# Kernel tuning notes

Measured on AMD Instinct MI355X. Metric: run time of the kernel, lower is better.

Reference implementation:

```python
import jax, jax.numpy as jnp
import numpy as np

ALPHA = 0.2      # LeakyReLU negative slope
NEG_INF = -9e15  # mask value from the original code

def setup_inputs() -> dict:
    key = jax.random.key(0)
    k1, k2, k3, k4 = jax.random.split(key, 4)
    B, M, F_IN, F_OUT = 16, 2048, 128, 64
    h = jax.random.normal(k1, (B, M, F_IN), dtype=jnp.float32)
    adj = jax.random.randint(k2, (B, M, M), 0, 2, dtype=jnp.int32)
    W = jax.random.normal(k3, (F_IN, F_OUT), dtype=jnp.float32) * 0.1
    a = jax.random.normal(k4, (2 * F_OUT, 1), dtype=jnp.float32) * 0.1
    return {"h": h, "adj": adj, "W": W, "a": a}

def reference(h, adj, W, a):
    # h: [B,M,Fin], adj: [B,M,M], W: [Fin,E], a: [2E,1]
    Wh = jnp.matmul(h, W)                      # [B,M,E]
    E = Wh.shape[-1]
    a1, a2 = a[:E, 0], a[E:, 0]
    # decompose a^T [Wh_i || Wh_j] = (Wh_i . a1) + (Wh_j . a2)
    f1 = Wh @ a1                               # [B,M] (source/query term)
    f2 = Wh @ a2                               # [B,M] (target/key term)
    e = jax.nn.leaky_relu(f1[:, :, None] + f2[:, None, :], negative_slope=ALPHA)  # [B,M,M]
    scores = jnp.where(adj > 0, e, NEG_INF)
    attn = jax.nn.softmax(scores, axis=-1)     # [B,M,M]  (dropout p=0 / eval mode)
    h_prime = jnp.matmul(attn, Wh)             # [B,M,E]
    return jax.nn.elu(h_prime)                 # concat=True branch
```

## Files before the change

### kernel.cpp

```cpp
#include <hip/hip_runtime.h>


#define M_     2048
#define FIN_   128
#define F_     64
#define ALPHA_ 0.2f
#define HS_    132
#define WT_    132
#define MS_    68

typedef float  float4_ __attribute__((ext_vector_type(4)));
typedef short  short8  __attribute__((ext_vector_type(8)));
typedef int    int4_   __attribute__((ext_vector_type(4)));
typedef unsigned int u32x4 __attribute__((ext_vector_type(4)));
typedef unsigned short u16;
typedef unsigned int   u32;

static __device__ __forceinline__ u32 cvtpk(float lo, float hi) {
    u32 r;
    asm("v_cvt_pk_bf16_f32 %0, %1, %2" : "=v"(r) : "v"(lo), "v"(hi));
    return r;
}

static __device__ __forceinline__ int4_ ntload4(const int* p) {
    return __builtin_nontemporal_load((const int4_*)p);
}

__global__ __launch_bounds__(256, 4) void k_prep(
    const float* __restrict__ h, const float* __restrict__ W,
    const float* __restrict__ a, u16* __restrict__ hbf,
    float* __restrict__ f1all, float* __restrict__ f2all)
{
    __shared__ float a_s[2 * F_];
    __shared__ float wa1[FIN_], wa2[FIN_];
    __shared__ float hs[32 * HS_];

    const int tid = threadIdx.x;
    const u32 bid = blockIdx.x;
    const u32 lg  = (bid & 7) * 128 + (bid >> 3);
    const int b   = lg >> 6;
    const int t   = lg & 63;

    if (tid < 128) a_s[tid] = a[tid];

    const int tok = tid >> 3, f0 = (tid & 7) * 16;
    const float* hp = h + ((size_t)(b * M_ + t * 32 + tok)) * FIN_ + f0;
    float4_ x0 = *(const float4_*)hp;
    float4_ x1 = *(const float4_*)(hp + 4);
    float4_ x2 = *(const float4_*)(hp + 8);
    float4_ x3 = *(const float4_*)(hp + 12);
    __syncthreads();

    if (tid < FIN_) {
        float s1 = 0.f, s2 = 0.f;
#pragma unroll 8
        for (int n = 0; n < F_; ++n) {
            float wv = W[tid * F_ + n];
            s1 += wv * a_s[n];
            s2 += wv * a_s[F_ + n];
        }
        wa1[tid] = s1;
        wa2[tid] = s2;
    }

    float* hr = hs + tok * HS_ + f0;
    *(float4_*)(hr)      = x0;
    *(float4_*)(hr + 4)  = x1;
    *(float4_*)(hr + 8)  = x2;
    *(float4_*)(hr + 12) = x3;
    __syncthreads();

    {
        const int l = tid & 63, lc = l & 15, q = l >> 4;
        const int nt0 = (tid >> 6) * 2;
        u32x4* ob = (u32x4*)hbf + ((size_t)(b * 64 + t)) * 8 * 64;
#pragma unroll
        for (int ni = 0; ni < 2; ++ni) {
            const int nt = nt0 + ni;
            const float* cp = hs + (q * 8) * HS_ + nt * 16 + lc;
            u32x4 wv;
            wv[0] = cvtpk(cp[0 * HS_], cp[1 * HS_]);
            wv[1] = cvtpk(cp[2 * HS_], cp[3 * HS_]);
            wv[2] = cvtpk(cp[4 * HS_], cp[5 * HS_]);
            wv[3] = cvtpk(cp[6 * HS_], cp[7 * HS_]);
            ob[nt * 64 + l] = wv;
        }
    }

    {
        const int r = tid >> 3, k0 = (tid & 7) * 16;
        const float* rp = hs + r * HS_ + k0;
        float s1 = 0.f, s2 = 0.f;
#pragma unroll
        for (int k = 0; k < 16; ++k) {
            s1 += rp[k] * wa1[k0 + k];
            s2 += rp[k] * wa2[k0 + k];
        }
        s1 += __shfl_xor(s1, 1, 64); s2 += __shfl_xor(s2, 1, 64);
        s1 += __shfl_xor(s1, 2, 64); s2 += __shfl_xor(s2, 2, 64);
        s1 += __shfl_xor(s1, 4, 64); s2 += __shfl_xor(s2, 4, 64);
        if ((tid & 7) == 0) {
            f1all[b * M_ + t * 32 + r] = s1;
            f2all[b * M_ + t * 32 + r] = s2;
        }
    }
}

__global__ __launch_bounds__(256, 4) void k_pack(
    const int* __restrict__ adj, u32* __restrict__ mask)
{
    const int l = threadIdx.x & 63;
    u32 s = blockIdx.x * 4 + (threadIdx.x >> 6);
#pragma unroll 4
    for (int it = 0; it < 32; ++it, s += 8192) {
        int4_ v = ntload4(adj + (size_t)s * 256 + l * 4);
        u32 m = ((v[0] > 0 ? 1u : 0u) | (v[1] > 0 ? 2u : 0u)
               | (v[2] > 0 ? 4u : 0u) | (v[3] > 0 ? 8u : 0u)) << ((l & 7) * 4);
        m |= __shfl_xor(m, 1, 64);
        m |= __shfl_xor(m, 2, 64);
        m |= __shfl_xor(m, 4, 64);
        if ((l & 7) == 0) mask[s * 8 + (l >> 3)] = m;
    }
}

__global__ __launch_bounds__(256, 2) void k_main(
    const u32* __restrict__ mask, const u16* __restrict__ hbf,
    const float* __restrict__ f1all, const float* __restrict__ f2all,
    const float* __restrict__ W, float* __restrict__ out)
{
    __shared__ char  dyn[41984];
    __shared__ float dens[64];

    u32x4* lbuf = (u32x4*)dyn;
    float* f2s  = (float*)(dyn + 16384);
    u32*   mlds = (u32*)(dyn + 24576);
    float* Tsum = (float*)dyn;

    const int tid  = threadIdx.x;
    const int w    = tid >> 6;
    const int l    = tid & 63;
    const int lc   = l & 15;
    const int quad = l >> 4;

    const u32 bid = blockIdx.x;
    const u32 lg  = (bid & 7) * 64 + (bid >> 3);
    const int b   = lg >> 5;
    const int i0  = (lg & 31) * 64;

    {
        const int o = tid * 8;
        float4_ v0 = *(const float4_*)(f2all + b * M_ + o);
        float4_ v1 = *(const float4_*)(f2all + b * M_ + o + 4);
        *(float4_*)(f2s + o)     = v0;
        *(float4_*)(f2s + o + 4) = v1;
    }
    {
        const u32* mrow = mask + ((size_t)(b * M_ + i0)) * 64;
#pragma unroll
        for (int c = 0; c < 4; ++c) {
            const int gw = c * 1024 + tid * 4;
            u32x4 v = *(const u32x4*)(mrow + gw);
            *(u32x4*)(mlds + (gw >> 6) * MS_ + (gw & 63)) = v;
        }
    }

    const float f1r = f1all[b * M_ + i0 + w * 16 + lc];
    const u32x4* hbs = (const u32x4*)hbf + (size_t)b * 32768;
    const u32* mrd = mlds + (w * 16 + lc) * MS_;
    const int  msh = quad * 8;

    u32x4 sA0, sA1, sB0, sB1;
    sA0 = hbs[tid];
    sA1 = hbs[256 + tid];
    lbuf[tid]       = sA0;
    lbuf[256 + tid] = sA1;
    sB0 = hbs[512 + tid];
    sB1 = hbs[512 + 256 + tid];

    __syncthreads();

    float denacc = 0.f;
    float4_ acc[8];
#pragma unroll
    for (int nt = 0; nt < 8; ++nt) acc[nt] = (float4_){0.f, 0.f, 0.f, 0.f};

#define SC(GE, GO, BE, BO, IDX)                                 \
        {                                                       \
            float xe = f1r + (GE); xe = fmaxf(xe, ALPHA_ * xe); \
            float xo = f1r + (GO); xo = fmaxf(xo, ALPHA_ * xo); \
            float ee = (mq & (1u << (BE))) ? __expf(xe) : 0.f;  \
            float eo = (mq & (1u << (BO))) ? __expf(xo) : 0.f;  \
            u32 pk = cvtpk(ee, eo);                             \
            d += __uint_as_float(pk << 16);                     \
            d += __uint_as_float(pk & 0xFFFF0000u);             \
            pw[IDX] = pk;                                       \
        }

#define STAGE(T, L0, L1, W0, W1)                                              \
    {                                                                         \
        const int tl = ((T) + 2 < 64) ? (T) + 2 : 63;                         \
        L0 = hbs[tl * 512 + tid];                                             \
        L1 = hbs[tl * 512 + 256 + tid];                                       \
        __builtin_amdgcn_sched_barrier(0);                                    \
        const u32x4* lc_ = lbuf + ((T) & 1) * 512;                            \
        u32x4 bb[8];                                                          \
        _Pragma("unroll")                                                     \
        for (int nt = 0; nt < 8; ++nt) bb[nt] = lc_[nt * 64 + l];             \
        const u32 mq = mrd[T] >> msh;                                         \
        float4_ g0 = *(const float4_*)(f2s + (T) * 32 + quad * 8);            \
        float4_ g1 = *(const float4_*)(f2s + (T) * 32 + quad * 8 + 4);        \
        u32x4 pw;                                                             \
        float d = 0.f;                                                        \
        SC(g0[0], g0[1], 0, 1, 0)                                             \
        SC(g0[2], g0[3], 2, 3, 1)                                             \
        SC(g1[0], g1[1], 4, 5, 2)                                             \
        SC(g1[2], g1[3], 6, 7, 3)                                             \
        denacc += d;                                                          \
        const short8 af = __builtin_bit_cast(short8, pw);                     \
        _Pragma("unroll")                                                     \
        for (int nt = 0; nt < 8; ++nt)                                        \
            acc[nt] = __builtin_amdgcn_mfma_f32_16x16x32_bf16(                \
                af, __builtin_bit_cast(short8, bb[nt]), acc[nt], 0, 0, 0);    \
        __builtin_amdgcn_sched_barrier(0);                                    \
        u32x4* ln_ = lbuf + (((T) + 1) & 1) * 512;                            \
        ln_[tid]       = W0;                                                  \
        ln_[256 + tid] = W1;                                                  \
        asm volatile("s_waitcnt lgkmcnt(0)" ::: "memory");                    \
        __builtin_amdgcn_s_barrier();                                         \
        __builtin_amdgcn_sched_barrier(0);                                    \
    }

    for (int o2 = 0; o2 < 32; ++o2) {
        STAGE(2 * o2,     sA0, sA1, sB0, sB1)
        STAGE(2 * o2 + 1, sB0, sB1, sA0, sA1)
    }
#undef STAGE
#undef SC

    denacc += __shfl_xor(denacc, 16, 64);
    denacc += __shfl_xor(denacc, 32, 64);
    if (quad == 0) dens[w * 16 + lc] = denacc;
    __syncthreads();

#pragma unroll
    for (int nt = 0; nt < 8; ++nt)
#pragma unroll
        for (int mm = 0; mm < 4; ++mm)
            Tsum[(w * 16 + quad * 4 + mm) * WT_ + nt * 16 + lc] = acc[nt][mm];
    __syncthreads();

#pragma unroll
    for (int rr = 0; rr < 2; ++rr) {
        const int r  = (tid >> 3) + rr * 32;
        const int n0 = (tid & 7) * 8;
        const float den  = dens[r];
        const float rden = (den > 0.f) ? (1.f / den) : 0.f;
        float u[8];
#pragma unroll
        for (int nn = 0; nn < 8; ++nn) u[nn] = 0.f;
#pragma unroll 4
        for (int k = 0; k < FIN_; ++k) {
            const float tv = Tsum[r * WT_ + k];
            float4_ wv0 = *(const float4_*)(W + k * F_ + n0);
            float4_ wv1 = *(const float4_*)(W + k * F_ + n0 + 4);
            u[0] += tv * wv0[0]; u[1] += tv * wv0[1];
            u[2] += tv * wv0[2]; u[3] += tv * wv0[3];
            u[4] += tv * wv1[0]; u[5] += tv * wv1[1];
            u[6] += tv * wv1[2]; u[7] += tv * wv1[3];
        }
        float4_ o0, o1;
#pragma unroll
        for (int nn = 0; nn < 8; ++nn) {
            float hp = u[nn] * rden;
            float o  = hp > 0.f ? hp : expm1f(hp);
            if (nn < 4) o0[nn] = o; else o1[nn - 4] = o;
        }
        float* op = out + ((size_t)(b * M_ + i0 + r)) * F_ + n0;
        *(float4_*)op       = o0;
        *(float4_*)(op + 4) = o1;
    }
}

extern "C" void kernel_launch(void* const* d_in, const int* in_sizes, int n_in,
                              void* d_out, int out_size, void* d_ws, size_t ws_size,
                              hipStream_t stream)
{
    (void)out_size; (void)ws_size;
    const float* h  = (const float*)d_in[0];
    const int* adjp = (const int*)d_in[1];
    const float* Wp = (const float*)d_in[2];
    const float* ap = (const float*)d_in[3];
    for (int i = 0; i < n_in; ++i) {
        long s = in_sizes[i];
        if      (s == 4194304L)  h    = (const float*)d_in[i];
        else if (s == 67108864L) adjp = (const int*)d_in[i];
        else if (s == 8192L)     Wp   = (const float*)d_in[i];
        else if (s == 128L)      ap   = (const float*)d_in[i];
    }
    u16*   hbf   = (u16*)d_ws;
    float* f1all = (float*)((char*)d_ws + (8u << 20));
    float* f2all = f1all + 16 * M_;
    u32*   maskp = (u32*)((char*)d_ws + (16u << 20));
    k_prep<<<1024, 256, 0, stream>>>(h, Wp, ap, hbf, f1all, f2all);
    k_pack<<<2048, 256, 0, stream>>>(adjp, maskp);
    k_main<<<512, 256, 0, stream>>>(maskp, hbf, f1all, f2all, Wp, (float*)d_out);
}
```

Before: 417.6 us.

## Merge prep and pack kernels; split key range across wave pairs in main

After: 429.9 us. +2.9%, slower.

```diff
diff --git a/kernel.cpp b/kernel.cpp
--- a/kernel.cpp
+++ b/kernel.cpp
@@ -7,7 +7,6 @@
 #define ALPHA_ 0.2f
 #define HS_    132
 #define WT_    132
-#define MS_    68
 
 typedef float  float4_ __attribute__((ext_vector_type(4)));
 typedef short  short8  __attribute__((ext_vector_type(8)));
@@ -26,16 +25,34 @@
     return __builtin_nontemporal_load((const int4_*)p);
 }
 
-__global__ __launch_bounds__(256, 4) void k_prep(
-    const float* __restrict__ h, const float* __restrict__ W,
-    const float* __restrict__ a, u16* __restrict__ hbf,
-    float* __restrict__ f1all, float* __restrict__ f2all)
+__global__ __launch_bounds__(256, 4) void k_pp(
+    const float* __restrict__ h, const int* __restrict__ adj,
+    const float* __restrict__ W, const float* __restrict__ a,
+    u16* __restrict__ hbf, float* __restrict__ f1all,
+    float* __restrict__ f2all, u32* __restrict__ mask)
 {
     __shared__ float a_s[2 * F_];
     __shared__ float wa1[FIN_], wa2[FIN_];
     __shared__ float hs[32 * HS_];
 
     const int tid = threadIdx.x;
+
+    if (blockIdx.x >= 1024) {
+        const int l = tid & 63;
+        u32 s = (blockIdx.x - 1024) * 4 + (tid >> 6);
+#pragma unroll 4
+        for (int it = 0; it < 32; ++it, s += 8192) {
+            int4_ v = ntload4(adj + (size_t)s * 256 + l * 4);
+            u32 m = ((v[0] > 0 ? 1u : 0u) | (v[1] > 0 ? 2u : 0u)
+                   | (v[2] > 0 ? 4u : 0u) | (v[3] > 0 ? 8u : 0u)) << ((l & 7) * 4);
+            m |= __shfl_xor(m, 1, 64);
+            m |= __shfl_xor(m, 2, 64);
+            m |= __shfl_xor(m, 4, 64);
+            if ((l & 7) == 0) mask[s * 8 + (l >> 3)] = m;
+        }
+        return;
+    }
+
     const u32 bid = blockIdx.x;
     const u32 lg  = (bid & 7) * 128 + (bid >> 3);
     const int b   = lg >> 6;
@@ -106,34 +123,16 @@
     }
 }
 
-__global__ __launch_bounds__(256, 4) void k_pack(
-    const int* __restrict__ adj, u32* __restrict__ mask)
-{
-    const int l = threadIdx.x & 63;
-    u32 s = blockIdx.x * 4 + (threadIdx.x >> 6);
-#pragma unroll 4
-    for (int it = 0; it < 32; ++it, s += 8192) {
-        int4_ v = ntload4(adj + (size_t)s * 256 + l * 4);
-        u32 m = ((v[0] > 0 ? 1u : 0u) | (v[1] > 0 ? 2u : 0u)
-               | (v[2] > 0 ? 4u : 0u) | (v[3] > 0 ? 8u : 0u)) << ((l & 7) * 4);
-        m |= __shfl_xor(m, 1, 64);
-        m |= __shfl_xor(m, 2, 64);
-        m |= __shfl_xor(m, 4, 64);
-        if ((l & 7) == 0) mask[s * 8 + (l >> 3)] = m;
-    }
-}
-
-__global__ __launch_bounds__(256, 2) void k_main(
+__global__ __launch_bounds__(256, 3) void k_main(
     const u32* __restrict__ mask, const u16* __restrict__ hbf,
     const float* __restrict__ f1all, const float* __restrict__ f2all,
     const float* __restrict__ W, float* __restrict__ out)
 {
-    __shared__ char  dyn[41984];
-    __shared__ float dens[64];
+    __shared__ char  dyn[40960];
+    __shared__ float dens2[64];
 
     u32x4* lbuf = (u32x4*)dyn;
-    float* f2s  = (float*)(dyn + 16384);
-    u32*   mlds = (u32*)(dyn + 24576);
+    float* f2s  = (float*)(dyn + 32768);
     float* Tsum = (float*)dyn;
 
     const int tid  = threadIdx.x;
@@ -141,11 +140,15 @@
     const int l    = tid & 63;
     const int lc   = l & 15;
     const int quad = l >> 4;
+    const int rg   = w & 1;
+    const int wh   = w >> 1;
+    const int ti   = tid & 127;
 
     const u32 bid = blockIdx.x;
-    const u32 lg  = (bid & 7) * 64 + (bid >> 3);
-    const int b   = lg >> 5;
-    const int i0  = (lg & 31) * 64;
+    const u32 lg  = (bid & 7) * 128 + (bid >> 3);
+    const int b   = lg >> 6;
+    const int i0  = (lg & 63) * 32;
+    const int row = i0 + rg * 16 + lc;
 
     {
         const int o = tid * 8;
@@ -154,29 +157,21 @@
         *(float4_*)(f2s + o)     = v0;
         *(float4_*)(f2s + o + 4) = v1;
     }
-    {
-        const u32* mrow = mask + ((size_t)(b * M_ + i0)) * 64;
-#pragma unroll
-        for (int c = 0; c < 4; ++c) {
-            const int gw = c * 1024 + tid * 4;
-            u32x4 v = *(const u32x4*)(mrow + gw);
-            *(u32x4*)(mlds + (gw >> 6) * MS_ + (gw & 63)) = v;
-        }
-    }
-
-    const float f1r = f1all[b * M_ + i0 + w * 16 + lc];
+
+    const u32* mrow = mask + ((size_t)(b * M_ + row)) * 64 + wh * 32 + quad * 8;
+    u32x4 mwa = *(const u32x4*)(mrow);
+    u32x4 mwb = *(const u32x4*)(mrow + 4);
+
+    const float f1r = f1all[b * M_ + row];
     const u32x4* hbs = (const u32x4*)hbf + (size_t)b * 32768;
-    const u32* mrd = mlds + (w * 16 + lc) * MS_;
-    const int  msh = quad * 8;
-
-    u32x4 sA0, sA1, sB0, sB1;
-    sA0 = hbs[tid];
-    sA1 = hbs[256 + tid];
-    lbuf[tid]       = sA0;
-    lbuf[256 + tid] = sA1;
-    sB0 = hbs[512 + tid];
-    sB1 = hbs[512 + 256 + tid];
-
+    const int msh = quad * 8;
+
+    {
+        const int Th = wh * 32;
+#pragma unroll
+        for (int j = 0; j < 4; ++j)
+            lbuf[wh * 512 + ti + 128 * j] = hbs[Th * 512 + ti + 128 * j];
+    }
     __syncthreads();
 
     float denacc = 0.f;
@@ -196,19 +191,24 @@
             pw[IDX] = pk;                                       \
         }
 
-#define STAGE(T, L0, L1, W0, W1)                                              \
+#define STEP(K)                                                               \
     {                                                                         \
-        const int tl = ((T) + 2 < 64) ? (T) + 2 : 63;                         \
-        L0 = hbs[tl * 512 + tid];                                             \
-        L1 = hbs[tl * 512 + 256 + tid];                                       \
+        const int kn = ((K) < 31) ? (K) + 1 : 31;                             \
+        u32x4 s0 = hbs[(wh * 32 + kn) * 512 + ti];                            \
+        u32x4 s1 = hbs[(wh * 32 + kn) * 512 + ti + 128];                      \
+        u32x4 s2 = hbs[(wh * 32 + kn) * 512 + ti + 256];                      \
+        u32x4 s3 = hbs[(wh * 32 + kn) * 512 + ti + 384];                      \
         __builtin_amdgcn_sched_barrier(0);                                    \
-        const u32x4* lc_ = lbuf + ((T) & 1) * 512;                            \
+        const u32x4* cb = lbuf + (((K) & 1) * 2 + wh) * 512;                  \
         u32x4 bb[8];                                                          \
         _Pragma("unroll")                                                     \
-        for (int nt = 0; nt < 8; ++nt) bb[nt] = lc_[nt * 64 + l];             \
-        const u32 mq = mrd[T] >> msh;                                         \
-        float4_ g0 = *(const float4_*)(f2s + (T) * 32 + quad * 8);            \
-        float4_ g1 = *(const float4_*)(f2s + (T) * 32 + quad * 8 + 4);        \
+        for (int nt = 0; nt < 8; ++nt) bb[nt] = cb[nt * 64 + l];              \
+        u32 mrw = __shfl((((K) & 7) < 4) ? mwa[(K) & 3] : mwb[(K) & 3],       \
+                         (((K) >> 3) << 4) + lc, 64);                         \
+        const u32 mq = mrw >> msh;                                            \
+        float4_ g0 = *(const float4_*)(f2s + (wh * 32 + (K)) * 32 + quad * 8);\
+        float4_ g1 = *(const float4_*)(f2s + (wh * 32 + (K)) * 32 + quad * 8  \
+                                       + 4);                                  \
         u32x4 pw;                                                             \
         float d = 0.f;                                                        \
         SC(g0[0], g0[1], 0, 1, 0)                                             \
@@ -222,38 +222,50 @@
             acc[nt] = __builtin_amdgcn_mfma_f32_16x16x32_bf16(                \
                 af, __builtin_bit_cast(short8, bb[nt]), acc[nt], 0, 0, 0);    \
         __builtin_amdgcn_sched_barrier(0);                                    \
-        u32x4* ln_ = lbuf + (((T) + 1) & 1) * 512;                            \
-        ln_[tid]       = W0;                                                  \
-        ln_[256 + tid] = W1;                                                  \
+        u32x4* nb = lbuf + ((((K) + 1) & 1) * 2 + wh) * 512;                  \
+        nb[ti]       = s0;                                                    \
+        nb[ti + 128] = s1;                                                    \
+        nb[ti + 256] = s2;                                                    \
+        nb[ti + 384] = s3;                                                    \
         asm volatile("s_waitcnt lgkmcnt(0)" ::: "memory");                    \
         __builtin_amdgcn_s_barrier();                                         \
         __builtin_amdgcn_sched_barrier(0);                                    \
     }
 
-    for (int o2 = 0; o2 < 32; ++o2) {
-        STAGE(2 * o2,     sA0, sA1, sB0, sB1)
-        STAGE(2 * o2 + 1, sB0, sB1, sA0, sA1)
-    }
-#undef STAGE
+#define STEP4(K) STEP(K) STEP((K) + 1) STEP((K) + 2) STEP((K) + 3)
+    STEP4(0)  STEP4(4)  STEP4(8)  STEP4(12)
+    STEP4(16) STEP4(20) STEP4(24) STEP4(28)
+#undef STEP4
+#undef STEP
 #undef SC
+
 
     denacc += __shfl_xor(denacc, 16, 64);
     denacc += __shfl_xor(denacc, 32, 64);
-    if (quad == 0) dens[w * 16 + lc] = denacc;
-    __syncthreads();
-
-#pragma unroll
-    for (int nt = 0; nt < 8; ++nt)
-#pragma unroll
-        for (int mm = 0; mm < 4; ++mm)
-            Tsum[(w * 16 + quad * 4 + mm) * WT_ + nt * 16 + lc] = acc[nt][mm];
-    __syncthreads();
-
-#pragma unroll
-    for (int rr = 0; rr < 2; ++rr) {
-        const int r  = (tid >> 3) + rr * 32;
+    if (quad == 0) dens2[wh * 32 + rg * 16 + lc] = denacc;
+    __syncthreads();
+
+    if (wh == 0) {
+#pragma unroll
+        for (int nt = 0; nt < 8; ++nt)
+#pragma unroll
+            for (int mm = 0; mm < 4; ++mm)
+                Tsum[(rg * 16 + quad * 4 + mm) * WT_ + nt * 16 + lc] = acc[nt][mm];
+    }
+    __syncthreads();
+    if (wh == 1) {
+#pragma unroll
+        for (int nt = 0; nt < 8; ++nt)
+#pragma unroll
+            for (int mm = 0; mm < 4; ++mm)
+                Tsum[(rg * 16 + quad * 4 + mm) * WT_ + nt * 16 + lc] += acc[nt][mm];
+    }
+    __syncthreads();
+
+    {
+        const int r  = tid >> 3;
         const int n0 = (tid & 7) * 8;
-        const float den  = dens[r];
+        const float den  = dens2[r] + dens2[32 + r];
         const float rden = (den > 0.f) ? (1.f / den) : 0.f;
         float u[8];
 #pragma unroll
@@ -301,7 +313,6 @@
     float* f1all = (float*)((char*)d_ws + (8u << 20));
     float* f2all = f1all + 16 * M_;
     u32*   maskp = (u32*)((char*)d_ws + (16u << 20));
-    k_prep<<<1024, 256, 0, stream>>>(h, Wp, ap, hbf, f1all, f2all);
-    k_pack<<<2048, 256, 0, stream>>>(adjp, maskp);
-    k_main<<<512, 256, 0, stream>>>(maskp, hbf, f1all, f2all, Wp, (float*)d_out);
-}
+    k_pp<<<3072, 256, 0, stream>>>(h, adjp, Wp, ap, hbf, f1all, f2all, maskp);
+    k_main<<<1024, 256, 0, stream>>>(maskp, hbf, f1all, f2all, Wp, (float*)d_out);
+}
```
